# Performance work log

Hardware: AMD Instinct MI355X
Metric: run time of the kernel (lower is better)

## Reference

```python
import jax, jax.numpy as jnp
import numpy as np

EPS = 1e-8  # torch cosine_similarity eps


def setup_inputs() -> dict:
    key = jax.random.key(0)
    kq, km = jax.random.split(key)
    B, N, D = 256, 100000, 1024
    query = jax.random.normal(kq, (B, D), dtype=jnp.float32)
    memory = jax.random.normal(km, (N, D), dtype=jnp.float32)
    return {"query": query, "memory": memory, "k": 16}


def reference(query, memory, k):
    # Batched, fused version of HierarchicalMemory.retrieve():
    # cosine similarity of each query against every stored module, then top-k.
    # sim(q, m) = q.m / max(||q||*||m||, eps), matching F.cosine_similarity.
    qn = jnp.linalg.norm(query, axis=-1)          # [B]
    mn = jnp.linalg.norm(memory, axis=-1)         # [N]
    dots = jnp.einsum("bd,nd->bn", query, memory)  # [B, N]
    sims = dots / jnp.maximum(qn[:, None] * mn[None, :], EPS)
    top_vals, top_idx = jax.lax.top_k(sims, k)    # [B, k] each
    return top_vals, top_idx
```

## Files before the change

kernel.cpp:

```cpp
#include <hip/hip_runtime.h>
#include <math.h>

#define DDIM 1024
#define BQ 256
#define EPSV 1e-8f
#define CH 4
#define TPC 32
#define NCAND (CH * TPC)

typedef short bf16x8 __attribute__((ext_vector_type(8)));
typedef float f32x4 __attribute__((ext_vector_type(4)));

__device__ __forceinline__ unsigned short f2bf(float x) {
  union { float f; unsigned int u; } v;
  v.f = x;
  unsigned int lsb = (v.u >> 16) & 1u;
  v.u += 0x7fffu + lsb;
  return (unsigned short)(v.u >> 16);
}
__device__ __forceinline__ float bf2f(unsigned short b) {
  union { unsigned int u; float f; } v;
  v.u = ((unsigned int)b) << 16;
  return v.f;
}
__device__ __forceinline__ unsigned int cvtpk_bf16(float lo, float hi) {
  unsigned int r;
  asm("v_cvt_pk_bf16_f32 %0, %1, %2" : "=v"(r) : "v"(lo), "v"(hi));
  return r;
}

#define ASYNC_CP16(gp, lp)                                                     \
  __builtin_amdgcn_global_load_lds(                                            \
      (const __attribute__((address_space(1))) unsigned int*)(const void*)(gp),\
      (__attribute__((address_space(3))) unsigned int*)(lp), 16, 0, 0)

__global__ __launch_bounds__(256) void prep_q(const float* __restrict__ Q,
                                              unsigned short* __restrict__ Qb,
                                              float* __restrict__ qn) {
  int wave = threadIdx.x >> 6, lane = threadIdx.x & 63;
  int q = blockIdx.x * 4 + wave;
  const float4* src = (const float4*)(Q + (size_t)q * DDIM);
  unsigned short* dst = Qb + (size_t)q * DDIM;
  float s = 0.f;
#pragma unroll
  for (int t = 0; t < 4; ++t) {
    float4 v = src[t * 64 + lane];
    s += v.x * v.x + v.y * v.y + v.z * v.z + v.w * v.w;
    ushort4 o;
    o.x = f2bf(v.x); o.y = f2bf(v.y); o.z = f2bf(v.z); o.w = f2bf(v.w);
    *(ushort4*)(dst + t * 256 + lane * 4) = o;
  }
#pragma unroll
  for (int o = 32; o > 0; o >>= 1) s += __shfl_down(s, o, 64);
  if (lane == 0) qn[q] = sqrtf(s);
}

__global__ __launch_bounds__(256) void gemm_topk(
    const float* __restrict__ M, const unsigned short* __restrict__ Qb,
    unsigned short* __restrict__ sims, float* __restrict__ rmn,
    int N, int Npitch) {
  __shared__ unsigned short Qs[2][256 * 32];
  __shared__ unsigned short Ms[2][64 * 32];
  const int tid = threadIdx.x;
  const int wave = tid >> 6, lane = tid & 63;
  const int quad = lane >> 4, l15 = lane & 15;
  const int n0 = blockIdx.x * 64;

  const int mrow = tid >> 2;
  const int mchunk = tid & 3;
  const bool mvalid = (n0 + mrow) < N;
  const float* mptr = M + (size_t)(mvalid ? (n0 + mrow) : 0) * DDIM + mchunk * 8;

  f32x4 acc[4][4];
#pragma unroll
  for (int i = 0; i < 4; ++i)
#pragma unroll
    for (int j = 0; j < 4; ++j) acc[i][j] = (f32x4){0.f, 0.f, 0.f, 0.f};
  float sumsq = 0.f;

  auto stageQ = [&](int k0, int buf) {
#pragma unroll
    for (int r = 0; r < 4; ++r) {
      int row0 = r * 64 + wave * 16;
      const unsigned short* g =
          Qb + (size_t)(row0 + (lane >> 2)) * DDIM + k0 + (lane & 3) * 8;
      ASYNC_CP16(g, &Qs[buf][row0 * 32]);
    }
  };

  stageQ(0, 0);
  float4 mrA0 = *(const float4*)(mptr);
  float4 mrA1 = *(const float4*)(mptr + 4);
  float4 mrB0 = *(const float4*)(mptr + 32);
  float4 mrB1 = *(const float4*)(mptr + 36);

  auto body = [&](int t, int buf, float4& r0, float4& r1) {
    sumsq += r0.x * r0.x + r0.y * r0.y + r0.z * r0.z + r0.w * r0.w +
             r1.x * r1.x + r1.y * r1.y + r1.z * r1.z + r1.w * r1.w;
    uint4 packed;
    packed.x = cvtpk_bf16(r0.x, r0.y);
    packed.y = cvtpk_bf16(r0.z, r0.w);
    packed.z = cvtpk_bf16(r1.x, r1.y);
    packed.w = cvtpk_bf16(r1.z, r1.w);
    *(uint4*)&Ms[buf][mrow * 32 + mchunk * 8] = packed;
    int k2 = t * 32 + 64;
    const float* p = mptr + ((k2 < DDIM) ? k2 : 0);
    r0 = *(const float4*)(p);
    r1 = *(const float4*)(p + 4);
    asm volatile("s_waitcnt vmcnt(2) lgkmcnt(0)" ::: "memory");
    __builtin_amdgcn_s_barrier();
    __builtin_amdgcn_sched_barrier(0);
    if (t < 31) stageQ(t * 32 + 32, buf ^ 1);
    bf16x8 afr[4], bfr[4];
#pragma unroll
    for (int i = 0; i < 4; ++i)
      afr[i] =
          *(const bf16x8*)&Qs[buf][(wave * 64 + i * 16 + l15) * 32 + quad * 8];
#pragma unroll
    for (int j = 0; j < 4; ++j)
      bfr[j] = *(const bf16x8*)&Ms[buf][(j * 16 + l15) * 32 + quad * 8];
#pragma unroll
    for (int i = 0; i < 4; ++i)
#pragma unroll
      for (int j = 0; j < 4; ++j)
        acc[i][j] = __builtin_amdgcn_mfma_f32_16x16x32_bf16(afr[i], bfr[j],
                                                            acc[i][j], 0, 0, 0);
  };

#pragma unroll 1
  for (int t = 0; t < 32; t += 2) {
    body(t, 0, mrA0, mrA1);
    body(t + 1, 1, mrB0, mrB1);
  }

  float s = sumsq;
  s += __shfl_xor(s, 1, 64);
  s += __shfl_xor(s, 2, 64);
  if (mchunk == 0) rmn[n0 + mrow] = (s > 0.f) ? rsqrtf(s) : 0.f;

#pragma unroll
  for (int i = 0; i < 4; ++i)
#pragma unroll
    for (int j = 0; j < 4; ++j)
#pragma unroll
      for (int r = 0; r < 4; ++r) {
        int q = wave * 64 + i * 16 + quad * 4 + r;
        int n = n0 + j * 16 + l15;
        sims[(size_t)q * Npitch + n] = f2bf(acc[i][j][r]);
      }
}

__device__ __forceinline__ bool better(float v1, int i1, float v2, int i2) {
  return v1 > v2 || (v1 == v2 && i1 < i2);
}

template <int L>
__device__ __forceinline__ void insert_topL(float (&tv)[L], int (&ti)[L],
                                            float v, int idx) {
  if (v > tv[L - 1] || (v == tv[L - 1] && idx < ti[L - 1])) {
    tv[L - 1] = v; ti[L - 1] = idx;
#pragma unroll
    for (int j = L - 1; j > 0; --j) {
      if (better(tv[j], ti[j], tv[j - 1], ti[j - 1])) {
        float fv = tv[j]; tv[j] = tv[j - 1]; tv[j - 1] = fv;
        int ii = ti[j]; ti[j] = ti[j - 1]; ti[j - 1] = ii;
      }
    }
  }
}

template <int L, typename F>
__device__ __forceinline__ void block_extract(float (&tv)[L], int (&ti)[L],
                                              int rounds, F&& emit) {
  __shared__ float s_v[4];
  __shared__ int s_i[4];
  __shared__ int s_t[4];
  __shared__ float s_wv;
  __shared__ int s_wi;
  __shared__ int s_wt;
  for (int r = 0; r < rounds; ++r) {
    float v = tv[0];
    int idx = ti[0];
    int src = threadIdx.x;
#pragma unroll
    for (int o = 32; o > 0; o >>= 1) {
      float ov = __shfl_down(v, o, 64);
      int oi = __shfl_down(idx, o, 64);
      int os = __shfl_down(src, o, 64);
      if (better(ov, oi, v, idx)) { v = ov; idx = oi; src = os; }
    }
    int lane = threadIdx.x & 63, w = threadIdx.x >> 6;
    if (lane == 0) { s_v[w] = v; s_i[w] = idx; s_t[w] = src; }
    __syncthreads();
    if (threadIdx.x == 0) {
      float bv = s_v[0]; int bi = s_i[0]; int bt = s_t[0];
      for (int w2 = 1; w2 < 4; ++w2)
        if (better(s_v[w2], s_i[w2], bv, bi)) { bv = s_v[w2]; bi = s_i[w2]; bt = s_t[w2]; }
      s_wv = bv; s_wi = bi; s_wt = bt;
    }
    __syncthreads();
    if (threadIdx.x == s_wt) {
#pragma unroll
      for (int j = 0; j < L - 1; ++j) { tv[j] = tv[j + 1]; ti[j] = ti[j + 1]; }
      tv[L - 1] = -INFINITY; ti[L - 1] = 0x7fffffff;
    }
    if (threadIdx.x == 0) emit(r, s_wv, s_wi);
    __syncthreads();
  }
}

__global__ __launch_bounds__(256) void select_chunks(
    const unsigned short* __restrict__ sims, const float* __restrict__ rmn,
    int* __restrict__ cand, int N, int Npitch, int Nc) {
  int q = blockIdx.y;
  int c = blockIdx.x;
  int start = c * Nc;
  int end = start + Nc;
  if (end > N) end = N;
  float tv[8]; int ti[8];
#pragma unroll
  for (int j = 0; j < 8; ++j) { tv[j] = -INFINITY; ti[j] = 0x7fffffff; }
  const unsigned short* row = sims + (size_t)q * Npitch;
  int base = start + threadIdx.x * 8;
  for (; base + 8 <= end; base += 2048) {
    uint4 wv = *(const uint4*)(row + base);
    float4 r0 = *(const float4*)&rmn[base];
    float4 r1 = *(const float4*)&rmn[base + 4];
    float f0 = bf2f((unsigned short)(wv.x & 0xffff)) * r0.x;
    float f1 = bf2f((unsigned short)(wv.x >> 16)) * r0.y;
    float f2 = bf2f((unsigned short)(wv.y & 0xffff)) * r0.z;
    float f3 = bf2f((unsigned short)(wv.y >> 16)) * r0.w;
    float f4 = bf2f((unsigned short)(wv.z & 0xffff)) * r1.x;
    float f5 = bf2f((unsigned short)(wv.z >> 16)) * r1.y;
    float f6 = bf2f((unsigned short)(wv.w & 0xffff)) * r1.z;
    float f7 = bf2f((unsigned short)(wv.w >> 16)) * r1.w;
    insert_topL<8>(tv, ti, f0, base + 0);
    insert_topL<8>(tv, ti, f1, base + 1);
    insert_topL<8>(tv, ti, f2, base + 2);
    insert_topL<8>(tv, ti, f3, base + 3);
    insert_topL<8>(tv, ti, f4, base + 4);
    insert_topL<8>(tv, ti, f5, base + 5);
    insert_topL<8>(tv, ti, f6, base + 6);
    insert_topL<8>(tv, ti, f7, base + 7);
  }
  if (base < end) {
    for (int n = base; n < end; ++n)
      insert_topL<8>(tv, ti, bf2f(row[n]) * rmn[n], n);
  }
  int* dst = cand + (size_t)q * NCAND + c * TPC;
  block_extract<8>(tv, ti, TPC, [&](int r, float v, int i) {
    dst[r] = (i == 0x7fffffff) ? 0 : i;
  });
}

__global__ __launch_bounds__(512) void rescore(
    const float* __restrict__ Q, const float* __restrict__ M,
    const float* __restrict__ qn, const int* __restrict__ cand,
    float* __restrict__ out, int N) {
  __shared__ float cosv[NCAND];
  __shared__ int cidx[NCAND];
  int q = blockIdx.x;
  int wave = threadIdx.x >> 6, lane = threadIdx.x & 63;
  const float4* qf4 = (const float4*)(Q + (size_t)q * DDIM);
  float4 qv[4];
#pragma unroll
  for (int t = 0; t < 4; ++t) qv[t] = qf4[t * 64 + lane];
  float qnv = qn[q];
#pragma unroll 1
  for (int i = 0; i < NCAND / 8; ++i) {
    int c = wave * (NCAND / 8) + i;
    int idx = cand[(size_t)q * NCAND + c];
    if (idx < 0 || idx >= N) idx = 0;
    const float4* mf4 = (const float4*)(M + (size_t)idx * DDIM);
    float dot = 0.f, sq = 0.f;
#pragma unroll
    for (int t = 0; t < 4; ++t) {
      float4 m = mf4[t * 64 + lane];
      dot += m.x * qv[t].x + m.y * qv[t].y + m.z * qv[t].z + m.w * qv[t].w;
      sq += m.x * m.x + m.y * m.y + m.z * m.z + m.w * m.w;
    }
#pragma unroll
    for (int o = 32; o > 0; o >>= 1) {
      dot += __shfl_down(dot, o, 64);
      sq += __shfl_down(sq, o, 64);
    }
    if (lane == 0) {
      cosv[c] = dot / fmaxf(qnv * sqrtf(sq), EPSV);
      cidx[c] = idx;
    }
  }
  __syncthreads();
  if (wave == 0) {
    float v0 = cosv[lane], v1 = cosv[lane + 64];
    int i0 = cidx[lane], i1 = cidx[lane + 64];
    for (int r = 0; r < 16; ++r) {
      bool fb = better(v0, i0, v1, i1);
      float bv = fb ? v0 : v1;
      int bi = fb ? i0 : i1;
      int bs = lane * 2 + (fb ? 0 : 1);
#pragma unroll
      for (int o = 32; o > 0; o >>= 1) {
        float ov = __shfl_down(bv, o, 64);
        int oi = __shfl_down(bi, o, 64);
        int os = __shfl_down(bs, o, 64);
        if (better(ov, oi, bv, bi)) { bv = ov; bi = oi; bs = os; }
      }
      bv = __shfl(bv, 0, 64);
      bi = __shfl(bi, 0, 64);
      bs = __shfl(bs, 0, 64);
      if (lane == (bs >> 1)) {
        if (bs & 1) v1 = -INFINITY; else v0 = -INFINITY;
      }
      if (lane == 0) {
        out[(size_t)q * 16 + r] = bv;
        out[(size_t)BQ * 16 + (size_t)q * 16 + r] = (float)bi;
      }
    }
  }
}

extern "C" void kernel_launch(void* const* d_in, const int* in_sizes, int n_in,
                              void* d_out, int out_size, void* d_ws, size_t ws_size,
                              hipStream_t stream) {
  const float* Q = (const float*)d_in[0];
  const float* M = (const float*)d_in[1];
  int N = in_sizes[1] / DDIM;
  float* out = (float*)d_out;

  int nb = (N + 63) / 64;
  int Npitch = nb * 64;

  char* w = (char*)d_ws;
  size_t off = 0;
  auto alloc = [&](size_t bytes) {
    char* p = w + off;
    off = (off + bytes + 255) & ~(size_t)255;
    return p;
  };
  unsigned short* Qb = (unsigned short*)alloc((size_t)BQ * DDIM * 2);
  float* qn = (float*)alloc((size_t)BQ * 4);
  float* rmn = (float*)alloc((size_t)Npitch * 4);
  int* cand = (int*)alloc((size_t)BQ * NCAND * 4);
  unsigned short* sims = (unsigned short*)alloc((size_t)BQ * Npitch * 2);
  (void)ws_size;

  int Nc = (((N + CH - 1) / CH) + 7) & ~7;

  prep_q<<<BQ / 4, 256, 0, stream>>>(Q, Qb, qn);
  gemm_topk<<<nb, 256, 0, stream>>>(M, Qb, sims, rmn, N, Npitch);
  select_chunks<<<dim3(CH, BQ), 256, 0, stream>>>(sims, rmn, cand, N, Npitch, Nc);
  rescore<<<BQ, 512, 0, stream>>>(Q, M, qn, cand, out, N);
}
```

Before: 722.7 us.

## Pre-swizzle query into MFMA fragment layout and load A operands directly to registers

The query prep kernel now writes bf16 queries in a fragment-ordered layout so each lane can load its MFMA A-operand with one 16-byte global load. The GEMM kernel drops the shared-memory Q staging buffer and async global-to-LDS copies, and instead double-buffers the A fragments in registers, prefetching the next K slice. This removes LDS traffic and LDS capacity for Q, which may raise occupancy. In exchange, every block re-reads Q from global/L2 per wave, raises register pressure, and the waitcnt no longer explicitly bounds vector memory loads before use, relying on the compiler.

```diff
diff --git a/kernel.cpp b/kernel.cpp
--- a/kernel.cpp
+++ b/kernel.cpp
@@ -29,26 +29,26 @@
   return r;
 }
 
-#define ASYNC_CP16(gp, lp)                                                     \
-  __builtin_amdgcn_global_load_lds(                                            \
-      (const __attribute__((address_space(1))) unsigned int*)(const void*)(gp),\
-      (__attribute__((address_space(3))) unsigned int*)(lp), 16, 0, 0)
-
 __global__ __launch_bounds__(256) void prep_q(const float* __restrict__ Q,
                                               unsigned short* __restrict__ Qb,
                                               float* __restrict__ qn) {
   int wave = threadIdx.x >> 6, lane = threadIdx.x & 63;
   int q = blockIdx.x * 4 + wave;
   const float4* src = (const float4*)(Q + (size_t)q * DDIM);
-  unsigned short* dst = Qb + (size_t)q * DDIM;
+  int g = q >> 4, qrow = q & 15;
   float s = 0.f;
 #pragma unroll
-  for (int t = 0; t < 4; ++t) {
-    float4 v = src[t * 64 + lane];
+  for (int t4 = 0; t4 < 4; ++t4) {
+    float4 v = src[t4 * 64 + lane];
     s += v.x * v.x + v.y * v.y + v.z * v.z + v.w * v.w;
+    int k = t4 * 256 + lane * 4;
+    int tt = k >> 5;
+    int kquad = (k >> 3) & 3;
+    int elem = k & 7;
+    size_t chunk = (size_t)(tt * 16 + g) * 64 + kquad * 16 + qrow;
     ushort4 o;
     o.x = f2bf(v.x); o.y = f2bf(v.y); o.z = f2bf(v.z); o.w = f2bf(v.w);
-    *(ushort4*)(dst + t * 256 + lane * 4) = o;
+    *(ushort4*)(Qb + chunk * 8 + elem) = o;
   }
 #pragma unroll
   for (int o = 32; o > 0; o >>= 1) s += __shfl_down(s, o, 64);
@@ -59,7 +59,6 @@
     const float* __restrict__ M, const unsigned short* __restrict__ Qb,
     unsigned short* __restrict__ sims, float* __restrict__ rmn,
     int N, int Npitch) {
-  __shared__ unsigned short Qs[2][256 * 32];
   __shared__ unsigned short Ms[2][64 * 32];
   const int tid = threadIdx.x;
   const int wave = tid >> 6, lane = tid & 63;
@@ -71,6 +70,8 @@
   const bool mvalid = (n0 + mrow) < N;
   const float* mptr = M + (size_t)(mvalid ? (n0 + mrow) : 0) * DDIM + mchunk * 8;
 
+  const bf16x8* qptr = (const bf16x8*)Qb + (size_t)wave * 256 + lane;
+
   f32x4 acc[4][4];
 #pragma unroll
   for (int i = 0; i < 4; ++i)
@@ -78,23 +79,16 @@
     for (int j = 0; j < 4; ++j) acc[i][j] = (f32x4){0.f, 0.f, 0.f, 0.f};
   float sumsq = 0.f;
 
-  auto stageQ = [&](int k0, int buf) {
-#pragma unroll
-    for (int r = 0; r < 4; ++r) {
-      int row0 = r * 64 + wave * 16;
-      const unsigned short* g =
-          Qb + (size_t)(row0 + (lane >> 2)) * DDIM + k0 + (lane & 3) * 8;
-      ASYNC_CP16(g, &Qs[buf][row0 * 32]);
-    }
-  };
-
-  stageQ(0, 0);
+  bf16x8 aA0 = qptr[0], aA1 = qptr[64], aA2 = qptr[128], aA3 = qptr[192];
+  bf16x8 aB0{}, aB1{}, aB2{}, aB3{};
   float4 mrA0 = *(const float4*)(mptr);
   float4 mrA1 = *(const float4*)(mptr + 4);
   float4 mrB0 = *(const float4*)(mptr + 32);
   float4 mrB1 = *(const float4*)(mptr + 36);
 
-  auto body = [&](int t, int buf, float4& r0, float4& r1) {
+  auto body = [&](int t, int buf, float4& r0, float4& r1, bf16x8& c0,
+                  bf16x8& c1, bf16x8& c2, bf16x8& c3, bf16x8& p0, bf16x8& p1,
+                  bf16x8& p2, bf16x8& p3) {
     sumsq += r0.x * r0.x + r0.y * r0.y + r0.z * r0.z + r0.w * r0.w +
              r1.x * r1.x + r1.y * r1.y + r1.z * r1.z + r1.w * r1.w;
     uint4 packed;
@@ -107,30 +101,37 @@
     const float* p = mptr + ((k2 < DDIM) ? k2 : 0);
     r0 = *(const float4*)(p);
     r1 = *(const float4*)(p + 4);
-    asm volatile("s_waitcnt vmcnt(2) lgkmcnt(0)" ::: "memory");
+    asm volatile("s_waitcnt lgkmcnt(0)" ::: "memory");
     __builtin_amdgcn_s_barrier();
     __builtin_amdgcn_sched_barrier(0);
-    if (t < 31) stageQ(t * 32 + 32, buf ^ 1);
-    bf16x8 afr[4], bfr[4];
-#pragma unroll
-    for (int i = 0; i < 4; ++i)
-      afr[i] =
-          *(const bf16x8*)&Qs[buf][(wave * 64 + i * 16 + l15) * 32 + quad * 8];
+    const bf16x8* qp = qptr + (size_t)((t + 1) & 31) * 1024;
+    p0 = qp[0]; p1 = qp[64]; p2 = qp[128]; p3 = qp[192];
+    bf16x8 bfr[4];
 #pragma unroll
     for (int j = 0; j < 4; ++j)
       bfr[j] = *(const bf16x8*)&Ms[buf][(j * 16 + l15) * 32 + quad * 8];
-#pragma unroll
-    for (int i = 0; i < 4; ++i)
-#pragma unroll
-      for (int j = 0; j < 4; ++j)
-        acc[i][j] = __builtin_amdgcn_mfma_f32_16x16x32_bf16(afr[i], bfr[j],
-                                                            acc[i][j], 0, 0, 0);
+    acc[0][0] = __builtin_amdgcn_mfma_f32_16x16x32_bf16(c0, bfr[0], acc[0][0], 0, 0, 0);
+    acc[0][1] = __builtin_amdgcn_mfma_f32_16x16x32_bf16(c0, bfr[1], acc[0][1], 0, 0, 0);
+    acc[0][2] = __builtin_amdgcn_mfma_f32_16x16x32_bf16(c0, bfr[2], acc[0][2], 0, 0, 0);
+    acc[0][3] = __builtin_amdgcn_mfma_f32_16x16x32_bf16(c0, bfr[3], acc[0][3], 0, 0, 0);
+    acc[1][0] = __builtin_amdgcn_mfma_f32_16x16x32_bf16(c1, bfr[0], acc[1][0], 0, 0, 0);
+    acc[1][1] = __builtin_amdgcn_mfma_f32_16x16x32_bf16(c1, bfr[1], acc[1][1], 0, 0, 0);
+    acc[1][2] = __builtin_amdgcn_mfma_f32_16x16x32_bf16(c1, bfr[2], acc[1][2], 0, 0, 0);
+    acc[1][3] = __builtin_amdgcn_mfma_f32_16x16x32_bf16(c1, bfr[3], acc[1][3], 0, 0, 0);
+    acc[2][0] = __builtin_amdgcn_mfma_f32_16x16x32_bf16(c2, bfr[0], acc[2][0], 0, 0, 0);
+    acc[2][1] = __builtin_amdgcn_mfma_f32_16x16x32_bf16(c2, bfr[1], acc[2][1], 0, 0, 0);
+    acc[2][2] = __builtin_amdgcn_mfma_f32_16x16x32_bf16(c2, bfr[2], acc[2][2], 0, 0, 0);
+    acc[2][3] = __builtin_amdgcn_mfma_f32_16x16x32_bf16(c2, bfr[3], acc[2][3], 0, 0, 0);
+    acc[3][0] = __builtin_amdgcn_mfma_f32_16x16x32_bf16(c3, bfr[0], acc[3][0], 0, 0, 0);
+    acc[3][1] = __builtin_amdgcn_mfma_f32_16x16x32_bf16(c3, bfr[1], acc[3][1], 0, 0, 0);
+    acc[3][2] = __builtin_amdgcn_mfma_f32_16x16x32_bf16(c3, bfr[2], acc[3][2], 0, 0, 0);
+    acc[3][3] = __builtin_amdgcn_mfma_f32_16x16x32_bf16(c3, bfr[3], acc[3][3], 0, 0, 0);
   };
 
 #pragma unroll 1
   for (int t = 0; t < 32; t += 2) {
-    body(t, 0, mrA0, mrA1);
-    body(t + 1, 1, mrB0, mrB1);
+    body(t, 0, mrA0, mrA1, aA0, aA1, aA2, aA3, aB0, aB1, aB2, aB3);
+    body(t + 1, 1, mrB0, mrB1, aB0, aB1, aB2, aB3, aA0, aA1, aA2, aA3);
   }
 
   float s = sumsq;
```

Result: faster. 705.3 us (-2.4%).
